# Kernel optimization log

Measured on AMD Instinct MI355X. Metric: run time of the kernel, lower is better.

The kernel has to match this reference:

```python
import jax, jax.numpy as jnp
import numpy as np

# fatigue class -> emotion target distribution; row 3 is the uniform fallback
_TABLE = np.array([
    [0.05, 0.02, 0.03, 0.4, 0.05, 0.4, 0.05],
    [0.05, 0.05, 0.05, 0.05, 0.3, 0.05, 0.45],
    [0.1, 0.15, 0.2, 0.02, 0.35, 0.03, 0.15],
    [1.0 / 7.0] * 7,
], dtype=np.float32)

B = 4_000_000

def setup_inputs() -> dict:
    key = jax.random.key(0)
    k1, k2, k3 = jax.random.split(key, 3)
    fatigue_logits = jax.random.normal(k1, (B, 3), dtype=jnp.float32)
    emotion_logits = jax.random.normal(k2, (B, 7), dtype=jnp.float32)
    fatigue_targets = jax.random.randint(k3, (B,), 0, 4, dtype=jnp.int64)
    return {"fatigue_logits": fatigue_logits,
            "emotion_logits": emotion_logits,
            "fatigue_targets": fatigue_targets}

def reference(fatigue_logits, emotion_logits, fatigue_targets):
    eps = 1e-8
    table = jnp.asarray(_TABLE)
    # targets outside {0,1,2} map to the uniform row (index 3)
    idx = jnp.where((fatigue_targets >= 0) & (fatigue_targets <= 2), fatigue_targets, 3)
    target = table[idx]                      # [B, 7] gather from tiny LUT
    target = target + eps
    target = target / jnp.sum(target, axis=-1, keepdims=True)
    probs = jax.nn.softmax(emotion_logits, axis=-1)
    log_input = jnp.log(probs + eps)
    # F.kl_div(log_input, target, reduction='batchmean')
    kl = jnp.sum(target * (jnp.log(target) - log_input)) / target.shape[0]
    return kl
```

## Files before the change

kernel.cpp:

```cpp
#include <hip/hip_runtime.h>
#include <cmath>

struct KLC {
    float w0[7], w1[7], w2[7], w3[7];
    float cst0, cst1, cst2, cst3;
};

typedef __attribute__((ext_vector_type(4))) float f4;
typedef __attribute__((ext_vector_type(4))) int   i4;

__device__ __forceinline__ void row_part(
    float x0, float x1, float x2, float x3, float x4, float x5, float x6,
    int t, const KLC& kc, float& lin, float& Z)
{
    int c = ((unsigned)t <= 2u) ? t : 3;

    Z = __expf(x0) + __expf(x1) + __expf(x2) + __expf(x3)
      + __expf(x4) + __expf(x5) + __expf(x6);

    float d0 = fmaf(kc.w0[6], x6, fmaf(kc.w0[5], x5, fmaf(kc.w0[4], x4,
               fmaf(kc.w0[3], x3, fmaf(kc.w0[2], x2, fmaf(kc.w0[1], x1, kc.w0[0] * x0))))));
    float d1 = fmaf(kc.w1[6], x6, fmaf(kc.w1[5], x5, fmaf(kc.w1[4], x4,
               fmaf(kc.w1[3], x3, fmaf(kc.w1[2], x2, fmaf(kc.w1[1], x1, kc.w1[0] * x0))))));
    float d2 = fmaf(kc.w2[6], x6, fmaf(kc.w2[5], x5, fmaf(kc.w2[4], x4,
               fmaf(kc.w2[3], x3, fmaf(kc.w2[2], x2, fmaf(kc.w2[1], x1, kc.w2[0] * x0))))));
    float d3 = fmaf(kc.w3[6], x6, fmaf(kc.w3[5], x5, fmaf(kc.w3[4], x4,
               fmaf(kc.w3[3], x3, fmaf(kc.w3[2], x2, fmaf(kc.w3[1], x1, kc.w3[0] * x0))))));

    float dw = (c == 0) ? d0 : (c == 1) ? d1 : (c == 2) ? d2 : d3;
    float cs = (c == 0) ? kc.cst0 : (c == 1) ? kc.cst1 : (c == 2) ? kc.cst2 : kc.cst3;
    lin = cs - dw;
}

__device__ __forceinline__ float quad_kl(
    f4 c0, f4 c1, f4 c2, f4 c3, f4 c4, f4 c5, f4 c6, i4 tq, const KLC& kc)
{
    float l0, l1, l2, l3, Z0, Z1, Z2, Z3;
    row_part(c0.x, c0.y, c0.z, c0.w, c1.x, c1.y, c1.z, tq.x, kc, l0, Z0);
    row_part(c1.w, c2.x, c2.y, c2.z, c2.w, c3.x, c3.y, tq.y, kc, l1, Z1);
    row_part(c3.z, c3.w, c4.x, c4.y, c4.z, c4.w, c5.x, tq.z, kc, l2, Z2);
    row_part(c5.y, c5.z, c5.w, c6.x, c6.y, c6.z, c6.w, tq.w, kc, l3, Z3);
    return l0 + l1 + l2 + l3 + __logf((Z0 * Z1) * (Z2 * Z3));
}

__global__ __launch_bounds__(256) void kl_main(
    const float* __restrict__ logits,
    const int*   __restrict__ tgt,
    int nchunks,
    double* __restrict__ partial,
    KLC kc)
{
    __shared__ f4 lds[4 * 448 + 4];
    const int lane = threadIdx.x & 63;
    const int wave = threadIdx.x >> 6;
    f4* const myl = &lds[wave * 448];

    const f4* __restrict__ lg = (const f4*)logits;
    const i4* __restrict__ tg = (const i4*)tgt;

    const int gwave  = blockIdx.x * 4 + wave;
    const int nwaves = gridDim.x * 4;

    float local = 0.0f;
    for (int ch = gwave; ch < nchunks; ch += nwaves) {
        asm volatile("s_waitcnt lgkmcnt(0)" ::: "memory");

        const long long base4 = (long long)ch * 448;
        #pragma unroll
        for (int k = 0; k < 7; ++k) {
            __builtin_amdgcn_global_load_lds(
                (const __attribute__((address_space(1))) void*)(lg + base4 + k * 64 + lane),
                (__attribute__((address_space(3))) void*)(myl + k * 64),
                16, 0, 0);
        }
        i4 tq = tg[(long long)ch * 64 + lane];

        asm volatile("s_waitcnt vmcnt(0)" ::: "memory");

        f4 c0 = myl[lane * 7 + 0];
        f4 c1 = myl[lane * 7 + 1];
        f4 c2 = myl[lane * 7 + 2];
        f4 c3 = myl[lane * 7 + 3];
        f4 c4 = myl[lane * 7 + 4];
        f4 c5 = myl[lane * 7 + 5];
        f4 c6 = myl[lane * 7 + 6];

        local += quad_kl(c0, c1, c2, c3, c4, c5, c6, tq, kc);
    }

    #pragma unroll
    for (int off = 32; off > 0; off >>= 1)
        local += __shfl_down(local, off, 64);

    __shared__ float smem[4];
    if (lane == 0) smem[wave] = local;
    __syncthreads();
    if (threadIdx.x == 0)
        partial[blockIdx.x] = (double)(smem[0] + smem[1] + smem[2] + smem[3]);
}

__global__ __launch_bounds__(256) void kl_reduce(
    const float* __restrict__ logits,
    const int*   __restrict__ tgt,
    long long tail_start, int tail,
    const double* __restrict__ partial, int nb,
    float* __restrict__ out, int B, KLC kc)
{
    double s = 0.0;
    for (int i = threadIdx.x; i < nb; i += 256) s += partial[i];

    float tl = 0.0f;
    for (int r = threadIdx.x; r < tail; r += 256) {
        const float* x = logits + (tail_start + r) * 7;
        float lin, Z;
        row_part(x[0], x[1], x[2], x[3], x[4], x[5], x[6],
                 tgt[tail_start + r], kc, lin, Z);
        tl += lin + __logf(Z);
    }
    s += (double)tl;

    #pragma unroll
    for (int off = 32; off > 0; off >>= 1)
        s += __shfl_down(s, off, 64);

    __shared__ double smem[4];
    int lane = threadIdx.x & 63;
    int wid  = threadIdx.x >> 6;
    if (lane == 0) smem[wid] = s;
    __syncthreads();
    if (threadIdx.x == 0)
        out[0] = (float)((smem[0] + smem[1] + smem[2] + smem[3]) / (double)B);
}

extern "C" void kernel_launch(void* const* d_in, const int* in_sizes, int n_in,
                              void* d_out, int out_size, void* d_ws, size_t ws_size,
                              hipStream_t stream) {
    const float* emotion = (const float*)d_in[1];
    const int*   targets = (const int*)d_in[2];
    float*  out     = (float*)d_out;
    double* partial = (double*)d_ws;

    const int B = in_sizes[2];
    const int nchunks = B / 256;
    const int tail = B - nchunks * 256;
    const long long tail_start = (long long)nchunks * 256;

    int nb = 1280;
    if ((size_t)nb * sizeof(double) > ws_size)
        nb = (int)(ws_size / sizeof(double));

    static const double T[4][7] = {
        {0.05, 0.02, 0.03, 0.4, 0.05, 0.4, 0.05},
        {0.05, 0.05, 0.05, 0.05, 0.3, 0.05, 0.45},
        {0.1, 0.15, 0.2, 0.02, 0.35, 0.03, 0.15},
        {1.0/7.0, 1.0/7.0, 1.0/7.0, 1.0/7.0, 1.0/7.0, 1.0/7.0, 1.0/7.0},
    };
    const double eps = 1e-8;
    KLC kc;
    float* wrows[4] = { kc.w0, kc.w1, kc.w2, kc.w3 };
    float* csts[4]  = { &kc.cst0, &kc.cst1, &kc.cst2, &kc.cst3 };
    for (int c = 0; c < 4; ++c) {
        double s = 0.0;
        for (int j = 0; j < 7; ++j) s += T[c][j] + eps;
        double cst = 0.0;
        for (int j = 0; j < 7; ++j) {
            double w = (T[c][j] + eps) / s;
            wrows[c][j] = (float)w;
            cst += w * std::log(w);
        }
        *csts[c] = (float)cst;
    }

    kl_main<<<nb, 256, 0, stream>>>(emotion, targets, nchunks, partial, kc);
    kl_reduce<<<1, 256, 0, stream>>>(emotion, targets, tail_start, tail,
                                     partial, nb, out, B, kc);
}
```

Measured before the change: 196.1 us.

## Double-buffer LDS loads and fuse final reduction via atomic ticket

```diff
diff --git a/kernel.cpp b/kernel.cpp
--- a/kernel.cpp
+++ b/kernel.cpp
@@ -43,93 +43,112 @@
     return l0 + l1 + l2 + l3 + __logf((Z0 * Z1) * (Z2 * Z3));
 }
 
-__global__ __launch_bounds__(256) void kl_main(
+__global__ __launch_bounds__(64) void kl_fused(
     const float* __restrict__ logits,
     const int*   __restrict__ tgt,
-    int nchunks,
-    double* __restrict__ partial,
-    KLC kc)
+    int nchunks, int nb,
+    long long tail_start, int tail,
+    double*   __restrict__ partial,
+    unsigned* __restrict__ ticket,
+    float*    __restrict__ out, int B, KLC kc)
 {
-    __shared__ f4 lds[4 * 448 + 4];
-    const int lane = threadIdx.x & 63;
-    const int wave = threadIdx.x >> 6;
-    f4* const myl = &lds[wave * 448];
+    __shared__ f4 lds[2 * 448];
+    const int lane = threadIdx.x;
+    const int w    = blockIdx.x;
 
     const f4* __restrict__ lg = (const f4*)logits;
     const i4* __restrict__ tg = (const i4*)tgt;
 
-    const int gwave  = blockIdx.x * 4 + wave;
-    const int nwaves = gridDim.x * 4;
+    float local = 0.0f;
+    const int iters = (nchunks - w + nb - 1) / nb;
 
-    float local = 0.0f;
-    for (int ch = gwave; ch < nchunks; ch += nwaves) {
+    int ch = w;
+    {
+        const f4* gp = lg + (long long)ch * 448 + lane;
+        #pragma unroll
+        for (int k = 0; k < 7; ++k)
+            __builtin_amdgcn_global_load_lds(
+                (const __attribute__((address_space(1))) void*)(gp + k * 64),
+                (__attribute__((address_space(3))) void*)(lds + k * 64),
+                16, 0, 0);
+    }
+    i4 tq_cur = tg[(long long)ch * 64 + lane];
+
+    int p = 0;
+    for (int t = 1; t < iters; ++t) {
+        const int chn = ch + nb;
         asm volatile("s_waitcnt lgkmcnt(0)" ::: "memory");
+        {
+            const f4* gp = lg + (long long)chn * 448 + lane;
+            f4* lb = lds + (p ^ 1) * 448;
+            #pragma unroll
+            for (int k = 0; k < 7; ++k)
+                __builtin_amdgcn_global_load_lds(
+                    (const __attribute__((address_space(1))) void*)(gp + k * 64),
+                    (__attribute__((address_space(3))) void*)(lb + k * 64),
+                    16, 0, 0);
+        }
+        i4 tq_next = tg[(long long)chn * 64 + lane];
 
-        const long long base4 = (long long)ch * 448;
-        #pragma unroll
-        for (int k = 0; k < 7; ++k) {
-            __builtin_amdgcn_global_load_lds(
-                (const __attribute__((address_space(1))) void*)(lg + base4 + k * 64 + lane),
-                (__attribute__((address_space(3))) void*)(myl + k * 64),
-                16, 0, 0);
-        }
-        i4 tq = tg[(long long)ch * 64 + lane];
+        asm volatile("s_waitcnt vmcnt(8)" ::: "memory");
 
-        asm volatile("s_waitcnt vmcnt(0)" ::: "memory");
-
-        f4 c0 = myl[lane * 7 + 0];
-        f4 c1 = myl[lane * 7 + 1];
-        f4 c2 = myl[lane * 7 + 2];
-        f4 c3 = myl[lane * 7 + 3];
-        f4 c4 = myl[lane * 7 + 4];
-        f4 c5 = myl[lane * 7 + 5];
-        f4 c6 = myl[lane * 7 + 6];
-
-        local += quad_kl(c0, c1, c2, c3, c4, c5, c6, tq, kc);
+        const f4* myl = lds + p * 448 + lane * 7;
+        local += quad_kl(myl[0], myl[1], myl[2], myl[3], myl[4], myl[5], myl[6],
+                         tq_cur, kc);
+        tq_cur = tq_next;
+        ch = chn;
+        p ^= 1;
+    }
+    asm volatile("s_waitcnt vmcnt(0)" ::: "memory");
+    {
+        const f4* myl = lds + p * 448 + lane * 7;
+        local += quad_kl(myl[0], myl[1], myl[2], myl[3], myl[4], myl[5], myl[6],
+                         tq_cur, kc);
     }
 
     #pragma unroll
     for (int off = 32; off > 0; off >>= 1)
         local += __shfl_down(local, off, 64);
 
-    __shared__ float smem[4];
-    if (lane == 0) smem[wave] = local;
-    __syncthreads();
-    if (threadIdx.x == 0)
-        partial[blockIdx.x] = (double)(smem[0] + smem[1] + smem[2] + smem[3]);
-}
+    int lastflag = 0;
+    if (lane == 0) {
+        __hip_atomic_store(&partial[w], (double)local,
+                           __ATOMIC_RELEASE, __HIP_MEMORY_SCOPE_AGENT);
+        unsigned old = __hip_atomic_fetch_add(ticket, 1u,
+                           __ATOMIC_ACQ_REL, __HIP_MEMORY_SCOPE_AGENT);
+        lastflag = (old == (unsigned)(nb - 1));
+    }
+    lastflag = __shfl(lastflag, 0, 64);
 
-__global__ __launch_bounds__(256) void kl_reduce(
-    const float* __restrict__ logits,
-    const int*   __restrict__ tgt,
-    long long tail_start, int tail,
-    const double* __restrict__ partial, int nb,
-    float* __restrict__ out, int B, KLC kc)
-{
-    double s = 0.0;
-    for (int i = threadIdx.x; i < nb; i += 256) s += partial[i];
+    if (lastflag) {
+        double s0 = 0.0, s1 = 0.0, s2 = 0.0, s3 = 0.0;
+        int i = lane;
+        for (; i + 192 < nb; i += 256) {
+            s0 += __hip_atomic_load(&partial[i      ], __ATOMIC_RELAXED, __HIP_MEMORY_SCOPE_AGENT);
+            s1 += __hip_atomic_load(&partial[i +  64], __ATOMIC_RELAXED, __HIP_MEMORY_SCOPE_AGENT);
+            s2 += __hip_atomic_load(&partial[i + 128], __ATOMIC_RELAXED, __HIP_MEMORY_SCOPE_AGENT);
+            s3 += __hip_atomic_load(&partial[i + 192], __ATOMIC_RELAXED, __HIP_MEMORY_SCOPE_AGENT);
+        }
+        for (; i < nb; i += 64)
+            s0 += __hip_atomic_load(&partial[i], __ATOMIC_RELAXED, __HIP_MEMORY_SCOPE_AGENT);
+        double s = (s0 + s1) + (s2 + s3);
 
-    float tl = 0.0f;
-    for (int r = threadIdx.x; r < tail; r += 256) {
-        const float* x = logits + (tail_start + r) * 7;
-        float lin, Z;
-        row_part(x[0], x[1], x[2], x[3], x[4], x[5], x[6],
-                 tgt[tail_start + r], kc, lin, Z);
-        tl += lin + __logf(Z);
+        float tl = 0.0f;
+        for (int r = lane; r < tail; r += 64) {
+            const float* x = logits + (tail_start + r) * 7;
+            float lin, Z;
+            row_part(x[0], x[1], x[2], x[3], x[4], x[5], x[6],
+                     tgt[tail_start + r], kc, lin, Z);
+            tl += lin + __logf(Z);
+        }
+        s += (double)tl;
+
+        #pragma unroll
+        for (int off = 32; off > 0; off >>= 1)
+            s += __shfl_down(s, off, 64);
+        if (lane == 0)
+            out[0] = (float)(s / (double)B);
     }
-    s += (double)tl;
-
-    #pragma unroll
-    for (int off = 32; off > 0; off >>= 1)
-        s += __shfl_down(s, off, 64);
-
-    __shared__ double smem[4];
-    int lane = threadIdx.x & 63;
-    int wid  = threadIdx.x >> 6;
-    if (lane == 0) smem[wid] = s;
-    __syncthreads();
-    if (threadIdx.x == 0)
-        out[0] = (float)((smem[0] + smem[1] + smem[2] + smem[3]) / (double)B);
 }
 
 extern "C" void kernel_launch(void* const* d_in, const int* in_sizes, int n_in,
@@ -139,15 +158,15 @@
     const int*   targets = (const int*)d_in[2];
     float*  out     = (float*)d_out;
     double* partial = (double*)d_ws;
+    unsigned* ticket = (unsigned*)((char*)d_ws + 32768);
 
     const int B = in_sizes[2];
     const int nchunks = B / 256;
     const int tail = B - nchunks * 256;
     const long long tail_start = (long long)nchunks * 256;
 
-    int nb = 1280;
-    if ((size_t)nb * sizeof(double) > ws_size)
-        nb = (int)(ws_size / sizeof(double));
+    int nb = 2048;
+    if (nb > nchunks) nb = nchunks;
 
     static const double T[4][7] = {
         {0.05, 0.02, 0.03, 0.4, 0.05, 0.4, 0.05},
@@ -171,7 +190,8 @@
         *csts[c] = (float)cst;
     }
 
-    kl_main<<<nb, 256, 0, stream>>>(emotion, targets, nchunks, partial, kc);
-    kl_reduce<<<1, 256, 0, stream>>>(emotion, targets, tail_start, tail,
-                                     partial, nb, out, B, kc);
+    hipMemsetAsync(ticket, 0, sizeof(unsigned), stream);
+    kl_fused<<<nb, 64, 0, stream>>>(emotion, targets, nchunks, nb,
+                                    tail_start, tail, partial, ticket,
+                                    out, B, kc);
 }
```

Result: slower. 272.6 us (+39.0%).
